# Kernel tuning notes

Hardware: AMD Instinct MI355X
Metric: run time of the kernel (lower is better)

## Reference

```python
import jax, jax.numpy as jnp
import numpy as np
import math

B, L, HD, H = 4, 1024, 512, 8
D = HD // H  # 64 per-head dim


def setup_inputs() -> dict:
    key = jax.random.key(0)
    ks = jax.random.split(key, 9)
    query = jax.random.normal(ks[0], (B, L, HD), jnp.float32)
    key_ = jax.random.normal(ks[1], (B, L, HD), jnp.float32)
    value = jax.random.normal(ks[2], (B, L, HD), jnp.float32)
    kernel = jax.random.normal(ks[3], (B * H, L, L), jnp.float32) * 0.1
    # sparse-ish boolean mask; low density so no row is fully masked
    attn_mask = jax.random.bernoulli(ks[4], 0.05, (B * H, L, L))
    in_proj_weight = jax.random.normal(ks[5], (3 * HD, HD), jnp.float32) * 0.02
    in_proj_bias = jnp.zeros((3 * HD,), jnp.float32)
    out_w = jax.random.normal(ks[6], (HD, HD), jnp.float32) * 0.02
    out_b = jnp.zeros((HD,), jnp.float32)
    return dict(query=query, key_=key_, value=value, attn_mask=attn_mask,
                key_padding_mask=0, kernel=kernel,
                in_proj_weight=in_proj_weight, in_proj_bias=in_proj_bias,
                out_w=out_w, out_b=out_b)


def _split_heads(x):
    # [B, L, HD] -> [B*H, L, D]
    b, l, _ = x.shape
    return x.reshape(b, l, H, D).transpose(0, 2, 1, 3).reshape(b * H, l, D)


def _merge_heads(x):
    # [B*H, L, D] -> [B, L, HD]
    bh, l, d = x.shape
    b = bh // H
    return x.reshape(b, H, l, d).transpose(0, 2, 1, 3).reshape(b, l, H * d)


def reference(query, key_, value, attn_mask, key_padding_mask, kernel,
              in_proj_weight, in_proj_bias, out_w, out_b):
    # key_padding_mask is falsy (None-equivalent) -> attn_mask unchanged
    wq, wk, wv = in_proj_weight[:HD], in_proj_weight[HD:2 * HD], in_proj_weight[2 * HD:]
    bq, bk, bv = in_proj_bias[:HD], in_proj_bias[HD:2 * HD], in_proj_bias[2 * HD:]
    q = _split_heads(query @ wq.T + bq)   # [B*H, L, D]
    k = _split_heads(key_ @ wk.T + bk)
    v = _split_heads(value @ wv.T + bv)
    scale = 1.0 / math.sqrt(D)
    scores = jnp.einsum('bqd,bkd->bqk', q, k) * scale  # [B*H, Lq, Lk]
    scores = scores + kernel.transpose(0, 2, 1)        # additive kernel bias
    scores = jnp.where(attn_mask, -jnp.inf, scores)    # masked_fill
    attn = jax.nn.softmax(scores, axis=-1)
    out = jnp.einsum('bqk,bkd->bqd', attn, v)          # [B*H, Lq, D]
    out = _merge_heads(out)                            # [B, Lq, HD]
    return out @ out_w.T + out_b
```

## Files before the change

kernel.cpp:

```cpp
#include <hip/hip_runtime.h>
#include <hip/hip_bf16.h>
#include <cstdint>
#include <cstddef>

typedef _Float16 half8 __attribute__((ext_vector_type(8)));
typedef _Float16 half4 __attribute__((ext_vector_type(4)));
typedef float f32x4 __attribute__((ext_vector_type(4)));

#define NB 4
#define NL 1024
#define NHD 512
#define NH 8
#define ND 64
#define NBH 32

#define MFMA16(a, b, c) __builtin_amdgcn_mfma_f32_16x16x32_f16((a), (b), (c), 0, 0, 0)

__global__ __launch_bounds__(256) void bitmask_kernel(
    const void* __restrict__ mask, unsigned* __restrict__ mb)
{
    __shared__ int s_byte;
    const int tid = threadIdx.x;
    const int t = blockIdx.x * 256 + tid;
    if (tid == 0) s_byte = 0;
    __syncthreads();

    const uint4* p = (const uint4*)((const unsigned char*)mask + (size_t)t * 32);
    uint4 a = p[0], b = p[1];
    unsigned src[8] = {a.x, a.y, a.z, a.w, b.x, b.y, b.z, b.w};
    int bad = 0;
#pragma unroll
    for (int j = 0; j < 8; ++j)
        if (src[j] != 0u && src[j] != 1u && src[j] != 0x3F800000u) bad = 1;
    if (bad) atomicOr(&s_byte, 1);
    __syncthreads();

    unsigned w = 0;
    if (s_byte) {
#pragma unroll
        for (int j = 0; j < 8; ++j) {
            unsigned u = src[j];
            w |= ((u & 0x000000FFu) ? 1u : 0u) << (4 * j + 0);
            w |= ((u & 0x0000FF00u) ? 1u : 0u) << (4 * j + 1);
            w |= ((u & 0x00FF0000u) ? 1u : 0u) << (4 * j + 2);
            w |= ((u & 0xFF000000u) ? 1u : 0u) << (4 * j + 3);
        }
    } else {
        const uint4* q = (const uint4*)((const unsigned*)mask + (size_t)t * 32);
#pragma unroll
        for (int j = 0; j < 8; ++j) {
            uint4 v = q[j];
            w |= (v.x ? 1u : 0u) << (4 * j + 0);
            w |= (v.y ? 1u : 0u) << (4 * j + 1);
            w |= (v.z ? 1u : 0u) << (4 * j + 2);
            w |= (v.w ? 1u : 0u) << (4 * j + 3);
        }
    }
    mb[t] = w;
}

__global__ __launch_bounds__(256) void qkv_gemm_kernel(
    const float* __restrict__ qin, const float* __restrict__ kin, const float* __restrict__ vin,
    const float* __restrict__ w, const float* __restrict__ bias,
    _Float16* __restrict__ qb, _Float16* __restrict__ kb, _Float16* __restrict__ vtb)
{
    const int mtile = blockIdx.x, ntile = blockIdx.y, proj = blockIdx.z;
    const float* A = proj == 0 ? qin : (proj == 1 ? kin : vin);
    const float* W = w + (size_t)proj * NHD * NHD;

    __shared__ __align__(16) _Float16 a_lds[128][72];
    __shared__ __align__(16) _Float16 b_lds[64][72];

    const int tid = threadIdx.x;
    const int wave = tid >> 6, lane = tid & 63, quad = lane >> 4, c = lane & 15;
    const int wm = wave >> 1, wn = wave & 1;

    f32x4 acc[4][2] = {};

    const int arow = tid >> 1, acol = (tid & 1) * 32;
    const int brow = tid >> 2, bcol = (tid & 3) * 16;
    const float* pa = &A[(size_t)(mtile * 128 + arow) * NHD + acol];
    const float* pb = &W[(size_t)(ntile * 64 + brow) * NHD + bcol];

    f32x4 ar[8], br[4];
#pragma unroll
    for (int j = 0; j < 8; ++j) ar[j] = *(const f32x4*)(pa + j * 4);
#pragma unroll
    for (int j = 0; j < 4; ++j) br[j] = *(const f32x4*)(pb + j * 4);

    for (int k0 = 0; k0 < NHD; k0 += 64) {
        half8 ah[4], bh_[2];
#pragma unroll
        for (int t = 0; t < 4; ++t)
#pragma unroll
            for (int j = 0; j < 4; ++j) {
                ah[t][j] = (_Float16)ar[2 * t][j];
                ah[t][4 + j] = (_Float16)ar[2 * t + 1][j];
            }
#pragma unroll
        for (int t = 0; t < 2; ++t)
#pragma unroll
            for (int j = 0; j < 4; ++j) {
                bh_[t][j] = (_Float16)br[2 * t][j];
                bh_[t][4 + j] = (_Float16)br[2 * t + 1][j];
            }
        __syncthreads();
#pragma unroll
        for (int t = 0; t < 4; ++t) *(half8*)&a_lds[arow][acol + t * 8] = ah[t];
#pragma unroll
        for (int t = 0; t < 2; ++t) *(half8*)&b_lds[brow][bcol + t * 8] = bh_[t];
        if (k0 < NHD - 64) {
            const float* na = pa + k0 + 64;
            const float* nb = pb + k0 + 64;
#pragma unroll
            for (int j = 0; j < 8; ++j) ar[j] = *(const f32x4*)(na + j * 4);
#pragma unroll
            for (int j = 0; j < 4; ++j) br[j] = *(const f32x4*)(nb + j * 4);
        }
        __syncthreads();

#pragma unroll
        for (int kk = 0; kk < 2; ++kk) {
            half8 af[4], bf[2];
#pragma unroll
            for (int ms = 0; ms < 4; ++ms)
                af[ms] = *(const half8*)&a_lds[wm * 64 + ms * 16 + c][kk * 32 + quad * 8];
#pragma unroll
            for (int ns = 0; ns < 2; ++ns)
                bf[ns] = *(const half8*)&b_lds[wn * 32 + ns * 16 + c][kk * 32 + quad * 8];
#pragma unroll
            for (int ms = 0; ms < 4; ++ms)
#pragma unroll
                for (int ns = 0; ns < 2; ++ns)
                    acc[ms][ns] = MFMA16(af[ms], bf[ns], acc[ms][ns]);
        }
    }

#pragma unroll
    for (int ms = 0; ms < 4; ++ms)
#pragma unroll
    for (int ns = 0; ns < 2; ++ns) {
        const int Cc = ntile * 64 + wn * 32 + ns * 16 + c;
        const float bv = bias[proj * NHD + Cc];
        const int h = Cc >> 6, d = Cc & 63;
#pragma unroll
        for (int r = 0; r < 4; ++r) {
            const int R = mtile * 128 + wm * 64 + ms * 16 + quad * 4 + r;
            const int b = R >> 10, l = R & 1023;
            const int bh = b * NH + h;
            float val = acc[ms][ns][r] + bv;
            if (proj == 0) {
                qb[((size_t)(bh * NL + l)) * ND + d] = (_Float16)(val * 0.125f);
            } else if (proj == 1) {
                kb[((size_t)(bh * NL + l)) * ND + d] = (_Float16)val;
            } else {
                vtb[((size_t)(bh * ND + d)) * NL + l] = (_Float16)val;
            }
        }
    }
}

__global__ __launch_bounds__(256) void attn_kernel(
    const _Float16* __restrict__ qb, const _Float16* __restrict__ kb, const _Float16* __restrict__ vtb,
    const float* __restrict__ kern, const unsigned* __restrict__ mb,
    _Float16* __restrict__ pO, float* __restrict__ pm, float* __restrict__ pl)
{
    const int qt = blockIdx.x, bh = blockIdx.y, half = blockIdx.z;
    const int tid = threadIdx.x, wave = tid >> 6, lane = tid & 63, quad = lane >> 4, c = lane & 15;
    const int q_base = qt * 64 + wave * 16;
    const int kt0 = half * 8;

    __shared__ __align__(16) _Float16 k_lds[64][72];
    __shared__ __align__(16) _Float16 vt_lds[64][72];
    __shared__ __align__(16) _Float16 p_lds[64][72];
    __shared__ __align__(16) float bias_lds[64][68];
    __shared__ unsigned mask_lds[64][2];

    half8 aq0 = *(const half8*)&qb[((size_t)(bh * NL) + q_base + c) * ND + quad * 8];
    half8 aq1 = *(const half8*)&qb[((size_t)(bh * NL) + q_base + c) * ND + 32 + quad * 8];

    f32x4 O[4] = {};
    float m_i[4] = {-1e30f, -1e30f, -1e30f, -1e30f};
    float l_i[4] = {0.f, 0.f, 0.f, 0.f};

    const int sr = tid >> 2, sc = (tid & 3) * 16;

    half8 kr0, kr1, vr0, vr1;
    f32x4 gr[4];
    unsigned mr = 0;

    {
        const _Float16* pk = &kb[((size_t)(bh * NL) + kt0 * 64 + sr) * ND + sc];
        kr0 = *(const half8*)pk; kr1 = *(const half8*)(pk + 8);
        const _Float16* pv = &vtb[((size_t)(bh * ND) + sr) * NL + kt0 * 64 + sc];
        vr0 = *(const half8*)pv; vr1 = *(const half8*)(pv + 8);
        const float* pg = &kern[((size_t)bh * NL + kt0 * 64 + sr) * NL + qt * 64 + sc];
#pragma unroll
        for (int j = 0; j < 4; ++j) gr[j] = *(const f32x4*)(pg + j * 4);
        if (tid < 128) mr = mb[((size_t)bh * NL + qt * 64 + (tid >> 1)) * 32 + kt0 * 2 + (tid & 1)];
    }

    for (int kt = 0; kt < 8; ++kt) {
        __syncthreads();
        *(half8*)&k_lds[sr][sc] = kr0;  *(half8*)&k_lds[sr][sc + 8] = kr1;
        *(half8*)&vt_lds[sr][sc] = vr0; *(half8*)&vt_lds[sr][sc + 8] = vr1;
#pragma unroll
        for (int j = 0; j < 4; ++j) *(f32x4*)&bias_lds[sr][(tid & 3) * 16 + j * 4] = gr[j];
        if (tid < 128) mask_lds[tid >> 1][tid & 1] = mr;

        if (kt < 7) {
            const int ktg = kt0 + kt + 1;
            const _Float16* pk = &kb[((size_t)(bh * NL) + ktg * 64 + sr) * ND + sc];
            kr0 = *(const half8*)pk; kr1 = *(const half8*)(pk + 8);
            const _Float16* pv = &vtb[((size_t)(bh * ND) + sr) * NL + ktg * 64 + sc];
            vr0 = *(const half8*)pv; vr1 = *(const half8*)(pv + 8);
            const float* pg = &kern[((size_t)bh * NL + ktg * 64 + sr) * NL + qt * 64 + sc];
#pragma unroll
            for (int j = 0; j < 4; ++j) gr[j] = *(const f32x4*)(pg + j * 4);
            if (tid < 128) mr = mb[((size_t)bh * NL + qt * 64 + (tid >> 1)) * 32 + ktg * 2 + (tid & 1)];
        }
        __syncthreads();

        f32x4 S[4];
#pragma unroll
        for (int ns = 0; ns < 4; ++ns) {
            f32x4 a = {};
            half8 bk0 = *(const half8*)&k_lds[ns * 16 + c][quad * 8];
            half8 bk1 = *(const half8*)&k_lds[ns * 16 + c][32 + quad * 8];
            a = MFMA16(aq0, bk0, a);
            a = MFMA16(aq1, bk1, a);
            S[ns] = a;
        }

        unsigned mw0[4], mw1[4];
#pragma unroll
        for (int r = 0; r < 4; ++r) {
            const int row = wave * 16 + quad * 4 + r;
            uint2 mm = *(const uint2*)&mask_lds[row][0];
            mw0[r] = mm.x; mw1[r] = mm.y;
        }

#pragma unroll
        for (int ns = 0; ns < 4; ++ns) {
            f32x4 bv = *(const f32x4*)&bias_lds[ns * 16 + c][wave * 16 + quad * 4];
            const int bit = ((ns & 1) << 4) + c;
#pragma unroll
            for (int r = 0; r < 4; ++r) {
                unsigned w = (ns < 2) ? mw0[r] : mw1[r];
                bool mk = (w >> bit) & 1u;
                S[ns][r] = mk ? -1e30f : (S[ns][r] + bv[r]);
            }
        }

        float pmax[4], al[4];
#pragma unroll
        for (int r = 0; r < 4; ++r) {
            float t = fmaxf(fmaxf(S[0][r], S[1][r]), fmaxf(S[2][r], S[3][r]));
            t = fmaxf(t, __shfl_xor(t, 1));
            t = fmaxf(t, __shfl_xor(t, 2));
            t = fmaxf(t, __shfl_xor(t, 4));
            t = fmaxf(t, __shfl_xor(t, 8));
            float mn = fmaxf(m_i[r], t);
            al[r] = __expf(m_i[r] - mn);
            m_i[r] = mn;
            pmax[r] = mn;
        }
        float rs[4] = {0.f, 0.f, 0.f, 0.f};
#pragma unroll
        for (int ns = 0; ns < 4; ++ns)
#pragma unroll
            for (int r = 0; r < 4; ++r) {
                float p = __expf(S[ns][r] - pmax[r]);
                S[ns][r] = p;
                rs[r] += p;
            }
#pragma unroll
        for (int r = 0; r < 4; ++r) {
            float t = rs[r];
            t += __shfl_xor(t, 1);
            t += __shfl_xor(t, 2);
            t += __shfl_xor(t, 4);
            t += __shfl_xor(t, 8);
            l_i[r] = l_i[r] * al[r] + t;
        }
#pragma unroll
        for (int ds = 0; ds < 4; ++ds)
#pragma unroll
            for (int r = 0; r < 4; ++r)
                O[ds][r] *= al[r];

#pragma unroll
        for (int ns = 0; ns < 4; ++ns)
#pragma unroll
            for (int r = 0; r < 4; ++r)
                p_lds[wave * 16 + quad * 4 + r][ns * 16 + c] = (_Float16)S[ns][r];
        __asm__ volatile("s_waitcnt lgkmcnt(0)" ::: "memory");

#pragma unroll
        for (int ks = 0; ks < 2; ++ks) {
            half8 ap = *(const half8*)&p_lds[wave * 16 + c][ks * 32 + quad * 8];
#pragma unroll
            for (int ds = 0; ds < 4; ++ds) {
                half8 bv = *(const half8*)&vt_lds[ds * 16 + c][ks * 32 + quad * 8];
                O[ds] = MFMA16(ap, bv, O[ds]);
            }
        }
    }

    const int ub = (bh * 16 + qt) * 2 + half;
    _Float16* pOb = pO + (size_t)ub * 4096;
#pragma unroll
    for (int ds = 0; ds < 4; ++ds)
#pragma unroll
        for (int r = 0; r < 4; ++r)
            pOb[(wave * 16 + quad * 4 + r) * 64 + ds * 16 + c] = (_Float16)O[ds][r];
    if (c == 0) {
#pragma unroll
        for (int r = 0; r < 4; ++r) {
            const int row = wave * 16 + quad * 4 + r;
            pm[(size_t)ub * 64 + row] = m_i[r];
            pl[(size_t)ub * 64 + row] = l_i[r];
        }
    }
}

__global__ __launch_bounds__(256) void out_gemm_kernel(
    const _Float16* __restrict__ pO, const float* __restrict__ pm, const float* __restrict__ pl,
    const float* __restrict__ w, const float* __restrict__ bias,
    float* __restrict__ out)
{
    const int mtile = blockIdx.x, ntile = blockIdx.y;
    const int bb = mtile >> 4, qt = mtile & 15;
    __shared__ __align__(16) _Float16 a_lds[64][72];
    __shared__ __align__(16) _Float16 b_lds[64][72];
    const int tid = threadIdx.x, wave = tid >> 6, lane = tid & 63, quad = lane >> 4, c = lane & 15;
    const int wm = wave >> 1, wn = wave & 1;
    f32x4 acc[2][2] = {};

    const int sr = tid >> 2, sc = (tid & 3) * 16;

    half8 p0a, p0b, p1a, p1b;
    f32x4 br[4];
    float m0, l0, m1, l1;

    auto fetch = [&](int k0) {
        const int h = k0 >> 6;
        const int u0 = ((bb * 8 + h) * 16 + qt) * 2;
        const _Float16* q0 = pO + (size_t)u0 * 4096 + sr * 64 + sc;
        p0a = *(const half8*)q0; p0b = *(const half8*)(q0 + 8);
        const _Float16* q1 = q0 + 4096;
        p1a = *(const half8*)q1; p1b = *(const half8*)(q1 + 8);
        m0 = pm[(size_t)u0 * 64 + sr]; l0 = pl[(size_t)u0 * 64 + sr];
        m1 = pm[(size_t)(u0 + 1) * 64 + sr]; l1 = pl[(size_t)(u0 + 1) * 64 + sr];
        const float* pb = &w[(size_t)(ntile * 64 + sr) * NHD + k0 + sc];
#pragma unroll
        for (int j = 0; j < 4; ++j) br[j] = *(const f32x4*)(pb + j * 4);
    };

    fetch(0);
    for (int k0 = 0; k0 < NHD; k0 += 64) {
        const float mx = fmaxf(m0, m1);
        const float e0 = __expf(m0 - mx), e1 = __expf(m1 - mx);
        const float linv = 1.0f / (l0 * e0 + l1 * e1);
        const float s0 = e0 * linv, s1 = e1 * linv;
        half8 ah0, ah1, bh0, bh1;
#pragma unroll
        for (int j = 0; j < 8; ++j) {
            ah0[j] = (_Float16)((float)p0a[j] * s0 + (float)p1a[j] * s1);
            ah1[j] = (_Float16)((float)p0b[j] * s0 + (float)p1b[j] * s1);
        }
#pragma unroll
        for (int j = 0; j < 4; ++j) {
            bh0[j] = (_Float16)br[0][j]; bh0[4 + j] = (_Float16)br[1][j];
            bh1[j] = (_Float16)br[2][j]; bh1[4 + j] = (_Float16)br[3][j];
        }
        __syncthreads();
        *(half8*)&a_lds[sr][sc] = ah0; *(half8*)&a_lds[sr][sc + 8] = ah1;
        *(half8*)&b_lds[sr][sc] = bh0; *(half8*)&b_lds[sr][sc + 8] = bh1;
        if (k0 < NHD - 64) fetch(k0 + 64);
        __syncthreads();

#pragma unroll
        for (int kk = 0; kk < 2; ++kk) {
            half8 af0 = *(const half8*)&a_lds[wm * 32 + c][kk * 32 + quad * 8];
            half8 af1 = *(const half8*)&a_lds[wm * 32 + 16 + c][kk * 32 + quad * 8];
            half8 bf0 = *(const half8*)&b_lds[wn * 32 + c][kk * 32 + quad * 8];
            half8 bf1 = *(const half8*)&b_lds[wn * 32 + 16 + c][kk * 32 + quad * 8];
            acc[0][0] = MFMA16(af0, bf0, acc[0][0]);
            acc[0][1] = MFMA16(af0, bf1, acc[0][1]);
            acc[1][0] = MFMA16(af1, bf0, acc[1][0]);
            acc[1][1] = MFMA16(af1, bf1, acc[1][1]);
        }
    }

#pragma unroll
    for (int ms = 0; ms < 2; ++ms)
#pragma unroll
    for (int ns = 0; ns < 2; ++ns) {
        const int Cc = ntile * 64 + wn * 32 + ns * 16 + c;
        const float bv = bias[Cc];
#pragma unroll
        for (int r = 0; r < 4; ++r) {
            const int R = mtile * 64 + wm * 32 + ms * 16 + quad * 4 + r;
            out[(size_t)R * NHD + Cc] = acc[ms][ns][r] + bv;
        }
    }
}

extern "C" void kernel_launch(void* const* d_in, const int* in_sizes, int n_in,
                              void* d_out, int out_size, void* d_ws, size_t ws_size,
                              hipStream_t stream)
{
    const float* query = (const float*)d_in[0];
    const float* key_  = (const float*)d_in[1];
    const float* value = (const float*)d_in[2];
    const void*  mask  = d_in[3];
    const float* kern  = (const float*)d_in[5];
    const float* ipw   = (const float*)d_in[6];
    const float* ipb   = (const float*)d_in[7];
    const float* outw  = (const float*)d_in[8];
    const float* outb  = (const float*)d_in[9];

    char* ws = (char*)d_ws;
    _Float16* qb  = (_Float16*)(ws);
    _Float16* kb  = (_Float16*)(ws + (4ull << 20));
    _Float16* vtb = (_Float16*)(ws + (8ull << 20));
    _Float16* pO  = (_Float16*)(ws + (16ull << 20));
    float* pm     = (float*)(ws + (32ull << 20));
    float* pl     = (float*)(ws + (33ull << 20));
    unsigned* mb  = (unsigned*)(ws + (40ull << 20));

    bitmask_kernel<<<4096, 256, 0, stream>>>(mask, mb);
    qkv_gemm_kernel<<<dim3(32, 8, 3), 256, 0, stream>>>(query, key_, value, ipw, ipb, qb, kb, vtb);
    attn_kernel<<<dim3(16, 32, 2), 256, 0, stream>>>(qb, kb, vtb, kern, mb, pO, pm, pl);
    out_gemm_kernel<<<dim3(64, 8), 256, 0, stream>>>(pO, pm, pl, outw, outb, (float*)d_out);
}
```

Before: 366.3 us.

## Pre-block kernel bias in prep pass and load it directly into registers

Merges the mask bitmask pass with a new pass that copies the 128MB fp32 kernel bias into a per-(bh, q-tile) blocked layout. The attention kernel can then read bias straight into registers in the MFMA output layout, dropping the bias LDS staging and its writes and reads. The second barrier moves to just after the LDS stores, so the next tile's global prefetch is issued after it. The cost is a full extra read and write of the 128MB bias tensor, which likely outweighs the LDS traffic saved.

```diff
diff --git a/kernel.cpp b/kernel.cpp
--- a/kernel.cpp
+++ b/kernel.cpp
@@ -16,47 +16,63 @@
 
 #define MFMA16(a, b, c) __builtin_amdgcn_mfma_f32_16x16x32_f16((a), (b), (c), 0, 0, 0)
 
-__global__ __launch_bounds__(256) void bitmask_kernel(
-    const void* __restrict__ mask, unsigned* __restrict__ mb)
+__global__ __launch_bounds__(256) void prep_kernel(
+    const float* __restrict__ kern, const void* __restrict__ mask,
+    float* __restrict__ kblk, unsigned* __restrict__ mb)
 {
-    __shared__ int s_byte;
     const int tid = threadIdx.x;
-    const int t = blockIdx.x * 256 + tid;
-    if (tid == 0) s_byte = 0;
-    __syncthreads();
-
-    const uint4* p = (const uint4*)((const unsigned char*)mask + (size_t)t * 32);
-    uint4 a = p[0], b = p[1];
-    unsigned src[8] = {a.x, a.y, a.z, a.w, b.x, b.y, b.z, b.w};
-    int bad = 0;
-#pragma unroll
-    for (int j = 0; j < 8; ++j)
-        if (src[j] != 0u && src[j] != 1u && src[j] != 0x3F800000u) bad = 1;
-    if (bad) atomicOr(&s_byte, 1);
-    __syncthreads();
-
-    unsigned w = 0;
-    if (s_byte) {
-#pragma unroll
-        for (int j = 0; j < 8; ++j) {
-            unsigned u = src[j];
-            w |= ((u & 0x000000FFu) ? 1u : 0u) << (4 * j + 0);
-            w |= ((u & 0x0000FF00u) ? 1u : 0u) << (4 * j + 1);
-            w |= ((u & 0x00FF0000u) ? 1u : 0u) << (4 * j + 2);
-            w |= ((u & 0xFF000000u) ? 1u : 0u) << (4 * j + 3);
-        }
+    if (blockIdx.x < 4096) {
+        __shared__ int s_byte;
+        const int t = blockIdx.x * 256 + tid;
+        if (tid == 0) s_byte = 0;
+        __syncthreads();
+
+        const uint4* p = (const uint4*)((const unsigned char*)mask + (size_t)t * 32);
+        uint4 a = p[0], b = p[1];
+        unsigned src[8] = {a.x, a.y, a.z, a.w, b.x, b.y, b.z, b.w};
+        int bad = 0;
+#pragma unroll
+        for (int j = 0; j < 8; ++j)
+            if (src[j] != 0u && src[j] != 1u && src[j] != 0x3F800000u) bad = 1;
+        if (bad) atomicOr(&s_byte, 1);
+        __syncthreads();
+
+        unsigned w = 0;
+        if (s_byte) {
+#pragma unroll
+            for (int j = 0; j < 8; ++j) {
+                unsigned u = src[j];
+                w |= ((u & 0x000000FFu) ? 1u : 0u) << (4 * j + 0);
+                w |= ((u & 0x0000FF00u) ? 1u : 0u) << (4 * j + 1);
+                w |= ((u & 0x00FF0000u) ? 1u : 0u) << (4 * j + 2);
+                w |= ((u & 0xFF000000u) ? 1u : 0u) << (4 * j + 3);
+            }
+        } else {
+            const uint4* q = (const uint4*)((const unsigned*)mask + (size_t)t * 32);
+#pragma unroll
+            for (int j = 0; j < 8; ++j) {
+                uint4 v = q[j];
+                w |= (v.x ? 1u : 0u) << (4 * j + 0);
+                w |= (v.y ? 1u : 0u) << (4 * j + 1);
+                w |= (v.z ? 1u : 0u) << (4 * j + 2);
+                w |= (v.w ? 1u : 0u) << (4 * j + 3);
+            }
+        }
+        mb[t] = w;
     } else {
-        const uint4* q = (const uint4*)((const unsigned*)mask + (size_t)t * 32);
-#pragma unroll
-        for (int j = 0; j < 8; ++j) {
-            uint4 v = q[j];
-            w |= (v.x ? 1u : 0u) << (4 * j + 0);
-            w |= (v.y ? 1u : 0u) << (4 * j + 1);
-            w |= (v.z ? 1u : 0u) << (4 * j + 2);
-            w |= (v.w ? 1u : 0u) << (4 * j + 3);
-        }
-    }
-    mb[t] = w;
+        const int bid2 = blockIdx.x - 4096;
+        unsigned ch = bid2 * 256 + tid;
+#pragma unroll
+        for (int i = 0; i < 16; ++i, ch += 524288) {
+            const unsigned c16 = ch & 255;
+            const unsigned k   = (ch >> 8) & 1023;
+            const unsigned bh  = ch >> 18;
+            const unsigned qt  = c16 >> 4;
+            const unsigned qq  = (c16 & 15) * 4;
+            f32x4 v = *(const f32x4*)(kern + (size_t)ch * 4);
+            *(f32x4*)(kblk + (((size_t)(bh * 16 + qt) * 1024) + k) * 64 + qq) = v;
+        }
+    }
 }
 
 __global__ __launch_bounds__(256) void qkv_gemm_kernel(
@@ -162,7 +178,7 @@
 
 __global__ __launch_bounds__(256) void attn_kernel(
     const _Float16* __restrict__ qb, const _Float16* __restrict__ kb, const _Float16* __restrict__ vtb,
-    const float* __restrict__ kern, const unsigned* __restrict__ mb,
+    const float* __restrict__ kblk, const unsigned* __restrict__ mb,
     _Float16* __restrict__ pO, float* __restrict__ pm, float* __restrict__ pl)
 {
     const int qt = blockIdx.x, bh = blockIdx.y, half = blockIdx.z;
@@ -173,7 +189,6 @@
     __shared__ __align__(16) _Float16 k_lds[64][72];
     __shared__ __align__(16) _Float16 vt_lds[64][72];
     __shared__ __align__(16) _Float16 p_lds[64][72];
-    __shared__ __align__(16) float bias_lds[64][68];
     __shared__ unsigned mask_lds[64][2];
 
     half8 aq0 = *(const half8*)&qb[((size_t)(bh * NL) + q_base + c) * ND + quad * 8];
@@ -186,27 +201,29 @@
     const int sr = tid >> 2, sc = (tid & 3) * 16;
 
     half8 kr0, kr1, vr0, vr1;
-    f32x4 gr[4];
     unsigned mr = 0;
+    f32x4 bias_r[4];
+
+    const float* bias_tile0 = kblk + ((size_t)(bh * 16 + qt) * 1024 + kt0 * 64) * 64;
+    const int bias_lane_off = c * 64 + wave * 16 + quad * 4;
 
     {
         const _Float16* pk = &kb[((size_t)(bh * NL) + kt0 * 64 + sr) * ND + sc];
         kr0 = *(const half8*)pk; kr1 = *(const half8*)(pk + 8);
         const _Float16* pv = &vtb[((size_t)(bh * ND) + sr) * NL + kt0 * 64 + sc];
         vr0 = *(const half8*)pv; vr1 = *(const half8*)(pv + 8);
-        const float* pg = &kern[((size_t)bh * NL + kt0 * 64 + sr) * NL + qt * 64 + sc];
-#pragma unroll
-        for (int j = 0; j < 4; ++j) gr[j] = *(const f32x4*)(pg + j * 4);
         if (tid < 128) mr = mb[((size_t)bh * NL + qt * 64 + (tid >> 1)) * 32 + kt0 * 2 + (tid & 1)];
+#pragma unroll
+        for (int ns = 0; ns < 4; ++ns)
+            bias_r[ns] = *(const f32x4*)(bias_tile0 + ns * 16 * 64 + bias_lane_off);
     }
 
     for (int kt = 0; kt < 8; ++kt) {
         __syncthreads();
         *(half8*)&k_lds[sr][sc] = kr0;  *(half8*)&k_lds[sr][sc + 8] = kr1;
         *(half8*)&vt_lds[sr][sc] = vr0; *(half8*)&vt_lds[sr][sc + 8] = vr1;
-#pragma unroll
-        for (int j = 0; j < 4; ++j) *(f32x4*)&bias_lds[sr][(tid & 3) * 16 + j * 4] = gr[j];
         if (tid < 128) mask_lds[tid >> 1][tid & 1] = mr;
+        __syncthreads();
 
         if (kt < 7) {
             const int ktg = kt0 + kt + 1;
@@ -214,12 +231,8 @@
             kr0 = *(const half8*)pk; kr1 = *(const half8*)(pk + 8);
             const _Float16* pv = &vtb[((size_t)(bh * ND) + sr) * NL + ktg * 64 + sc];
             vr0 = *(const half8*)pv; vr1 = *(const half8*)(pv + 8);
-            const float* pg = &kern[((size_t)bh * NL + ktg * 64 + sr) * NL + qt * 64 + sc];
-#pragma unroll
-            for (int j = 0; j < 4; ++j) gr[j] = *(const f32x4*)(pg + j * 4);
             if (tid < 128) mr = mb[((size_t)bh * NL + qt * 64 + (tid >> 1)) * 32 + ktg * 2 + (tid & 1)];
         }
-        __syncthreads();
 
         f32x4 S[4];
 #pragma unroll
@@ -242,14 +255,20 @@
 
 #pragma unroll
         for (int ns = 0; ns < 4; ++ns) {
-            f32x4 bv = *(const f32x4*)&bias_lds[ns * 16 + c][wave * 16 + quad * 4];
             const int bit = ((ns & 1) << 4) + c;
 #pragma unroll
             for (int r = 0; r < 4; ++r) {
                 unsigned w = (ns < 2) ? mw0[r] : mw1[r];
                 bool mk = (w >> bit) & 1u;
-                S[ns][r] = mk ? -1e30f : (S[ns][r] + bv[r]);
-            }
+                S[ns][r] = mk ? -1e30f : (S[ns][r] + bias_r[ns][r]);
+            }
+        }
+
+        if (kt < 7) {
+            const float* bt = bias_tile0 + (size_t)(kt + 1) * 64 * 64;
+#pragma unroll
+            for (int ns = 0; ns < 4; ++ns)
+                bias_r[ns] = *(const f32x4*)(bt + ns * 16 * 64 + bias_lane_off);
         }
 
         float pmax[4], al[4];
@@ -429,9 +448,10 @@
     float* pm     = (float*)(ws + (32ull << 20));
     float* pl     = (float*)(ws + (33ull << 20));
     unsigned* mb  = (unsigned*)(ws + (40ull << 20));
-
-    bitmask_kernel<<<4096, 256, 0, stream>>>(mask, mb);
+    float* kblk   = (float*)(ws + (48ull << 20));
+
+    prep_kernel<<<6144, 256, 0, stream>>>(kern, mask, kblk, mb);
     qkv_gemm_kernel<<<dim3(32, 8, 3), 256, 0, stream>>>(query, key_, value, ipw, ipb, qb, kb, vtb);
-    attn_kernel<<<dim3(16, 32, 2), 256, 0, stream>>>(qb, kb, vtb, kern, mb, pO, pm, pl);
+    attn_kernel<<<dim3(16, 32, 2), 256, 0, stream>>>(qb, kb, vtb, kblk, mb, pO, pm, pl);
     out_gemm_kernel<<<dim3(64, 8), 256, 0, stream>>>(pO, pm, pl, outw, outb, (float*)d_out);
 }
```

Measured after the change: 424.6 us. 1.16x slower.
